# Kernel optimization log

Measured on AMD Instinct MI355X. Metric: run time of the kernel, lower is better.

Reference implementation:

```python
import jax, jax.numpy as jnp
import numpy as np

T, B, NIN, NOUT, NLAYER = 512, 32, 512, 1024, 2


def setup_inputs() -> dict:
    key = jax.random.key(0)
    ks = jax.random.split(key, 7)
    s = 0.02
    return {
        "x": jax.random.normal(ks[0], (T, B, NIN), dtype=jnp.float32),
        "h0": jax.random.normal(ks[1], (NLAYER, B, NOUT), dtype=jnp.float32),
        "c0": jax.random.normal(ks[2], (NLAYER, B, NOUT), dtype=jnp.float32),
        "W0": jax.random.normal(ks[3], (4 * NOUT, NIN + NOUT), dtype=jnp.float32) * s,
        "b0": jax.random.normal(ks[4], (4 * NOUT,), dtype=jnp.float32) * s,
        "W1": jax.random.normal(ks[5], (4 * NOUT, NOUT + NOUT), dtype=jnp.float32) * s,
        "b1": jax.random.normal(ks[6], (4 * NOUT,), dtype=jnp.float32) * s,
    }


def _cell(xt, ht, ct, W, b):
    # xt: [B, nin_l], ht/ct: [B, nout]
    z = jnp.concatenate([xt, ht], axis=1) @ W.T + b  # [B, 4*nout]
    g1, g2, g3, o = jnp.split(z, 4, axis=1)
    g1 = jax.nn.sigmoid(g1)
    g2 = jax.nn.sigmoid(g2)
    g3 = jax.nn.sigmoid(g3)
    o = jnp.tanh(o)
    ct1 = ct * g1 + o * g2
    ht1 = jnp.tanh(ct1) * g3
    return ht1, ct1


def reference(x, h0, c0, W0, b0, W1, b1):
    Ws, bs = (W0, W1), (b0, b1)

    def step(carry, xt):
        hs, cs = carry  # tuples of [B, nout]
        new_hs, new_cs = [], []
        inp = xt
        for i in range(NLAYER):
            h1, c1 = _cell(inp, hs[i], cs[i], Ws[i], bs[i])
            new_hs.append(h1)
            new_cs.append(c1)
            inp = h1
        return (tuple(new_hs), tuple(new_cs)), inp

    init = (tuple(h0[i] for i in range(NLAYER)), tuple(c0[i] for i in range(NLAYER)))
    _, outputs = jax.lax.scan(step, init, x)  # [T, B, nout]
    # Faithful to source: returns the ORIGINAL (h0, c0), not the final state.
    return outputs, (h0, c0)
```

## Files before the change

kernel.cpp:

```cpp
#include <hip/hip_runtime.h>
#include <hip/hip_bf16.h>

#define TSTEPS 512
#define BATCH  32
#define NIN    512
#define NH     1024
#define BNH    (BATCH * NH)

typedef __attribute__((ext_vector_type(8))) short  short8v;
typedef __attribute__((ext_vector_type(4))) float  float4v;
typedef unsigned long long ull;

__device__ __forceinline__ unsigned short f2bf(float f) {
  return __builtin_bit_cast(unsigned short, __float2bfloat16(f));
}
__device__ __forceinline__ float4v mfma16(short8v a, short8v b, float4v c) {
  return __builtin_amdgcn_mfma_f32_16x16x32_bf16(a, b, c, 0, 0, 0);
}

__device__ __forceinline__ int swzh(int b, int k) {
  return (k >> 5) * 1024 + (b >> 4) * 512 + ((k >> 2) & 1) * 256 +
         (((b & 15) | (((k >> 3) & 3) << 4)) << 2) + (k & 3);
}
__device__ __forceinline__ int swzx(int b, int k) {
  return (k >> 5) * 1024 + (b >> 4) * 512 +
         (((b & 15) | (((k >> 3) & 3) << 4)) << 3) + (k & 7);
}

template<bool X16>
__device__ __forceinline__ void kpart8(const ushort* __restrict__ base, int kgb,
                                       int lane, const short8v (&wreg)[8][2],
                                       float4v (&acc)[2][2]) {
  if constexpr (X16) {
    short8v f[2][8];
#pragma unroll
    for (int mt = 0; mt < 2; ++mt)
#pragma unroll
      for (int q = 0; q < 8; ++q)
        f[mt][q] = *(const short8v*)(base + (size_t)(kgb + q) * 1024 + mt * 512 + lane * 8);
#pragma unroll
    for (int q = 0; q < 8; ++q)
#pragma unroll
      for (int mt = 0; mt < 2; ++mt) {
        acc[mt][0] = mfma16(f[mt][q], wreg[q][0], acc[mt][0]);
        acc[mt][1] = mfma16(f[mt][q], wreg[q][1], acc[mt][1]);
      }
  } else {
    ull lo[2][8], hi[2][8];
#pragma unroll
    for (int mt = 0; mt < 2; ++mt)
#pragma unroll
      for (int q = 0; q < 8; ++q) {
        const ull* p = (const ull*)(base + (size_t)(kgb + q) * 1024 + mt * 512 + lane * 4);
        lo[mt][q] = __hip_atomic_load(p,      __ATOMIC_RELAXED, __HIP_MEMORY_SCOPE_SYSTEM);
        hi[mt][q] = __hip_atomic_load(p + 64, __ATOMIC_RELAXED, __HIP_MEMORY_SCOPE_SYSTEM);
      }
#pragma unroll
    for (int q = 0; q < 8; ++q)
#pragma unroll
      for (int mt = 0; mt < 2; ++mt) {
        union { ull u[2]; short8v v; } cv;
        cv.u[0] = lo[mt][q]; cv.u[1] = hi[mt][q];
        acc[mt][0] = mfma16(cv.v, wreg[q][0], acc[mt][0]);
        acc[mt][1] = mfma16(cv.v, wreg[q][1], acc[mt][1]);
      }
  }
}

__device__ __forceinline__ void wave_poll(const int* __restrict__ flags,
                                          int base, int cnt, int need, int lane) {
  if (need <= 0) return;
  const int* f = flags + (size_t)(base + (lane & (cnt - 1))) * 4;
  while (!__all(__hip_atomic_load(f, __ATOMIC_RELAXED, __HIP_MEMORY_SCOPE_SYSTEM) >= need)) {}
  asm volatile("" ::: "memory");
}

__global__ __launch_bounds__(512, 2)
void lstm_rs(const float* __restrict__ c0_in,
             const float* __restrict__ W0, const float* __restrict__ b0_,
             const float* __restrict__ W1, const float* __restrict__ b1_,
             const ushort* __restrict__ xbf,
             ushort* __restrict__ ring0,
             ushort* __restrict__ ring1,
             int* __restrict__ flags,
             float* __restrict__ out) {
  __shared__ float zl[8][32][33];

  const int wg    = blockIdx.x;
  const int tid   = threadIdx.x;
  const int res   = wg & 7;
  const int layer = res >> 2;
  const int rank  = (wg >> 3) * 4 + (res & 3);
  const int j0    = rank * 8;
  const int K     = layer ? (2 * NH) : (NIN + NH);
  const float* W    = layer ? W1 : W0;
  const float* bias = layer ? b1_ : b0_;

  const int wv = tid >> 6, lane = tid & 63;
  const bool kactive = layer ? true : (wv < 6);

  short8v wreg[8][2];
  if (kactive) {
    const int wkbase = wv * 256;
#pragma unroll
    for (int q = 0; q < 8; ++q)
#pragma unroll
      for (int nt = 0; nt < 2; ++nt) {
        int n  = nt * 16 + (lane & 15);
        int gr = (n >> 3) * NH + j0 + (n & 7);
        int k  = wkbase + q * 32 + (lane >> 4) * 8;
        const float* p = W + (size_t)gr * K + k;
        float4 f0 = *(const float4*)p;
        float4 f1 = *(const float4*)(p + 4);
        short8v r;
        r[0] = (short)f2bf(f0.x); r[1] = (short)f2bf(f0.y);
        r[2] = (short)f2bf(f0.z); r[3] = (short)f2bf(f0.w);
        r[4] = (short)f2bf(f1.x); r[5] = (short)f2bf(f1.y);
        r[6] = (short)f2bf(f1.z); r[7] = (short)f2bf(f1.w);
        wreg[q][nt] = r;
      }
  } else {
#pragma unroll
    for (int q = 0; q < 8; ++q) { wreg[q][0] = short8v{}; wreg[q][1] = short8v{}; }
  }

  for (int i = lane; i < 32 * 33; i += 64) (&zl[wv][0][0])[i] = 0.f;

  const int bb = tid >> 3, jj = tid & 7;
  float c = 0.f, bg0 = 0.f, bg1 = 0.f, bg2 = 0.f, bg3 = 0.f;
  if (tid < 256) {
    bg0 = bias[0 * NH + j0 + jj];
    bg1 = bias[1 * NH + j0 + jj];
    bg2 = bias[2 * NH + j0 + jj];
    bg3 = bias[3 * NH + j0 + jj];
    c   = c0_in[layer * BNH + bb * NH + j0 + jj];
  }

  __syncthreads();

  for (int it = 0; it < TSTEPS; ++it) {
    float4v acc[2][2] = {{{0,0,0,0},{0,0,0,0}},{{0,0,0,0},{0,0,0,0}}};

    if (layer == 0) {
      if (wv < 2) {
        kpart8<true>(xbf + (size_t)it * 16384, 8 * wv, lane, wreg, acc);
      } else if (wv < 6) {
        wave_poll(flags, 32 * (wv - 2), 32, it, lane);
        kpart8<false>(ring0 + (size_t)(it & 7) * BNH, 8 * (wv - 2), lane, wreg, acc);
      } else {
        wave_poll(flags, 128 + 64 * (wv - 6), 64, it - 6, lane);
      }
    } else {
      if (wv < 4) {
        wave_poll(flags, 32 * wv, 32, it + 1, lane);
        kpart8<false>(ring0 + (size_t)((it + 1) & 7) * BNH, 8 * wv, lane, wreg, acc);
      } else {
        wave_poll(flags, 128 + 32 * (wv - 4), 32, it, lane);
        kpart8<false>(ring1 + (size_t)((it + 1) & 1) * BNH, 8 * (wv - 4), lane, wreg, acc);
      }
    }

    if (kactive) {
#pragma unroll
      for (int mt = 0; mt < 2; ++mt)
#pragma unroll
        for (int nt = 0; nt < 2; ++nt)
#pragma unroll
          for (int r = 0; r < 4; ++r)
            zl[wv][mt * 16 + (lane >> 4) * 4 + r][nt * 16 + (lane & 15)] = acc[mt][nt][r];
    }
    __syncthreads();

    if (tid < 256) {
      float zg[4];
#pragma unroll
      for (int g = 0; g < 4; ++g) {
        float s = 0.f;
#pragma unroll
        for (int w = 0; w < 8; ++w) s += zl[w][bb][g * 8 + jj];
        zg[g] = s;
      }
      float g1 = 1.f / (1.f + __expf(-(zg[0] + bg0)));
      float g2 = 1.f / (1.f + __expf(-(zg[1] + bg1)));
      float g3 = 1.f / (1.f + __expf(-(zg[2] + bg2)));
      float o  = tanhf(zg[3] + bg3);
      c = c * g1 + o * g2;
      float h = tanhf(c) * g3;
      unsigned short hb = f2bf(h);
      int so = swzh(bb, j0 + jj);
      if (layer == 0) {
        __hip_atomic_store(&ring0[(size_t)((it + 1) & 7) * BNH + so], hb,
                           __ATOMIC_RELAXED, __HIP_MEMORY_SCOPE_SYSTEM);
      } else {
        __hip_atomic_store(&ring1[(size_t)(it & 1) * BNH + so], hb,
                           __ATOMIC_RELAXED, __HIP_MEMORY_SCOPE_SYSTEM);
        out[(size_t)it * BNH + bb * NH + j0 + jj] = h;
      }
    }
    asm volatile("s_waitcnt vmcnt(0)" ::: "memory");
    __syncthreads();
    if (tid == 0) {
      __hip_atomic_store(&flags[(size_t)(layer * 128 + rank) * 4], it + 1,
                         __ATOMIC_RELAXED, __HIP_MEMORY_SCOPE_SYSTEM);
    }
  }
}

__global__ void prep(const float* __restrict__ x,
                     const float* __restrict__ h0_in, const float* __restrict__ c0_in,
                     ushort* __restrict__ xbf, ushort* __restrict__ ring0,
                     ushort* __restrict__ ring1, int* __restrict__ flags,
                     float* __restrict__ out) {
  int i = blockIdx.x * blockDim.x + threadIdx.x;
  {
    int t = i >> 14, rem = i & 16383;
    int b = rem >> 9, k = rem & 511;
    xbf[(size_t)t * 16384 + swzx(b, k)] = f2bf(x[i]);
  }
  if (i < BNH) {
    int b = i >> 10, j = i & 1023;
    int so = swzh(b, j);
    __hip_atomic_store(&ring0[so], f2bf(h0_in[i]),
                       __ATOMIC_RELAXED, __HIP_MEMORY_SCOPE_SYSTEM);
    __hip_atomic_store(&ring1[BNH + so], f2bf(h0_in[BNH + i]),
                       __ATOMIC_RELAXED, __HIP_MEMORY_SCOPE_SYSTEM);
  }
  if (i < 1024) {
    __hip_atomic_store(&flags[i], 0, __ATOMIC_RELAXED, __HIP_MEMORY_SCOPE_SYSTEM);
  }
  if (i < 2 * BNH) {
    const size_t TB = (size_t)TSTEPS * BNH;
    out[TB + i]           = h0_in[i];
    out[TB + 2 * BNH + i] = c0_in[i];
  }
}

extern "C" void kernel_launch(void* const* d_in, const int* in_sizes, int n_in,
                              void* d_out, int out_size, void* d_ws, size_t ws_size,
                              hipStream_t stream) {
  const float* x  = (const float*)d_in[0];
  const float* h0 = (const float*)d_in[1];
  const float* c0 = (const float*)d_in[2];
  const float* W0 = (const float*)d_in[3];
  const float* b0 = (const float*)d_in[4];
  const float* W1 = (const float*)d_in[5];
  const float* b1 = (const float*)d_in[6];
  float* out = (float*)d_out;

  ushort* xbf   = (ushort*)d_ws;
  ushort* ring0 = (ushort*)((char*)d_ws + 16777216);
  ushort* ring1 = (ushort*)((char*)d_ws + 17301504);
  int*    flags = (int*)((char*)d_ws + 17432576);

  prep<<<dim3(32768), dim3(256), 0, stream>>>(x, h0, c0, xbf, ring0, ring1, flags, out);

  void* args[] = {(void*)&c0, (void*)&W0, (void*)&b0, (void*)&W1, (void*)&b1,
                  (void*)&xbf, (void*)&ring0, (void*)&ring1, (void*)&flags, (void*)&out};
  (void)hipLaunchCooperativeKernel((const void*)lstm_rs, dim3(256), dim3(512),
                                   args, 0, stream);
}
```

Before: 2.778 ms.

## Replace ring buffers with full-history buffer and block-level flag polling

Layer 0 hidden states now go into a full per-timestep bf16 buffer instead of an 8-slot ring, and layer 1 reads its own previous output straight from the fp32 output tensor, converting on the fly. The x-to-bf16 prep pass is dropped; x is read as fp32 and converted inside the recurrent kernel. Per-wave polling with atomic loads is replaced by one wave polling all 128 flags with s_sleep, followed by a block barrier, and flags are spaced 64 bytes apart to cut contention. The change removes the big prep kernel and the ring-slot throttle between layers, at the cost of extra fp32 loads and conversions on the critical path and a barrier per step.

```diff
diff --git a/kernel.cpp b/kernel.cpp
--- a/kernel.cpp
+++ b/kernel.cpp
@@ -9,7 +9,6 @@
 
 typedef __attribute__((ext_vector_type(8))) short  short8v;
 typedef __attribute__((ext_vector_type(4))) float  float4v;
-typedef unsigned long long ull;
 
 __device__ __forceinline__ unsigned short f2bf(float f) {
   return __builtin_bit_cast(unsigned short, __float2bfloat16(f));
@@ -18,73 +17,83 @@
   return __builtin_amdgcn_mfma_f32_16x16x32_bf16(a, b, c, 0, 0, 0);
 }
 
-__device__ __forceinline__ int swzh(int b, int k) {
-  return (k >> 5) * 1024 + (b >> 4) * 512 + ((k >> 2) & 1) * 256 +
-         (((b & 15) | (((k >> 3) & 3) << 4)) << 2) + (k & 3);
-}
 __device__ __forceinline__ int swzx(int b, int k) {
   return (k >> 5) * 1024 + (b >> 4) * 512 +
          (((b & 15) | (((k >> 3) & 3) << 4)) << 3) + (k & 7);
 }
 
-template<bool X16>
-__device__ __forceinline__ void kpart8(const ushort* __restrict__ base, int kgb,
+__device__ __forceinline__ short8v cvt8(float4 f0, float4 f1) {
+  short8v r;
+  r[0] = (short)f2bf(f0.x); r[1] = (short)f2bf(f0.y);
+  r[2] = (short)f2bf(f0.z); r[3] = (short)f2bf(f0.w);
+  r[4] = (short)f2bf(f1.x); r[5] = (short)f2bf(f1.y);
+  r[6] = (short)f2bf(f1.z); r[7] = (short)f2bf(f1.w);
+  return r;
+}
+
+__device__ __forceinline__ void kpartB(const ushort* __restrict__ base, int kgb,
                                        int lane, const short8v (&wreg)[8][2],
                                        float4v (&acc)[2][2]) {
-  if constexpr (X16) {
-    short8v f[2][8];
-#pragma unroll
-    for (int mt = 0; mt < 2; ++mt)
-#pragma unroll
-      for (int q = 0; q < 8; ++q)
-        f[mt][q] = *(const short8v*)(base + (size_t)(kgb + q) * 1024 + mt * 512 + lane * 8);
+  short8v f[2][8];
+#pragma unroll
+  for (int mt = 0; mt < 2; ++mt)
 #pragma unroll
     for (int q = 0; q < 8; ++q)
-#pragma unroll
-      for (int mt = 0; mt < 2; ++mt) {
-        acc[mt][0] = mfma16(f[mt][q], wreg[q][0], acc[mt][0]);
-        acc[mt][1] = mfma16(f[mt][q], wreg[q][1], acc[mt][1]);
-      }
-  } else {
-    ull lo[2][8], hi[2][8];
-#pragma unroll
-    for (int mt = 0; mt < 2; ++mt)
-#pragma unroll
-      for (int q = 0; q < 8; ++q) {
-        const ull* p = (const ull*)(base + (size_t)(kgb + q) * 1024 + mt * 512 + lane * 4);
-        lo[mt][q] = __hip_atomic_load(p,      __ATOMIC_RELAXED, __HIP_MEMORY_SCOPE_SYSTEM);
-        hi[mt][q] = __hip_atomic_load(p + 64, __ATOMIC_RELAXED, __HIP_MEMORY_SCOPE_SYSTEM);
-      }
-#pragma unroll
-    for (int q = 0; q < 8; ++q)
-#pragma unroll
-      for (int mt = 0; mt < 2; ++mt) {
-        union { ull u[2]; short8v v; } cv;
-        cv.u[0] = lo[mt][q]; cv.u[1] = hi[mt][q];
-        acc[mt][0] = mfma16(cv.v, wreg[q][0], acc[mt][0]);
-        acc[mt][1] = mfma16(cv.v, wreg[q][1], acc[mt][1]);
-      }
-  }
-}
-
-__device__ __forceinline__ void wave_poll(const int* __restrict__ flags,
-                                          int base, int cnt, int need, int lane) {
+      f[mt][q] = *(const short8v*)(base + (size_t)(kgb + q) * 1024 + mt * 512 + lane * 8);
+#pragma unroll
+  for (int q = 0; q < 8; ++q)
+#pragma unroll
+    for (int mt = 0; mt < 2; ++mt) {
+      acc[mt][0] = mfma16(f[mt][q], wreg[q][0], acc[mt][0]);
+      acc[mt][1] = mfma16(f[mt][q], wreg[q][1], acc[mt][1]);
+    }
+}
+
+template<int RS>
+__device__ __forceinline__ void kpartF(const float* __restrict__ base, int kgb,
+                                       int lane, const short8v (&wreg)[8][2],
+                                       float4v (&acc)[2][2]) {
+  const int r0 = lane & 15, koff = (lane >> 4) * 8;
+  short8v f[2][8];
+#pragma unroll
+  for (int mt = 0; mt < 2; ++mt)
+#pragma unroll
+    for (int q = 0; q < 8; ++q) {
+      const float* p = base + (size_t)(mt * 16 + r0) * RS + (kgb + q) * 32 + koff;
+      f[mt][q] = cvt8(*(const float4*)p, *(const float4*)(p + 4));
+    }
+#pragma unroll
+  for (int q = 0; q < 8; ++q)
+#pragma unroll
+    for (int mt = 0; mt < 2; ++mt) {
+      acc[mt][0] = mfma16(f[mt][q], wreg[q][0], acc[mt][0]);
+      acc[mt][1] = mfma16(f[mt][q], wreg[q][1], acc[mt][1]);
+    }
+}
+
+__device__ __forceinline__ void poll128(const int* __restrict__ flags, int base,
+                                        int need, int lane) {
   if (need <= 0) return;
-  const int* f = flags + (size_t)(base + (lane & (cnt - 1))) * 4;
-  while (!__all(__hip_atomic_load(f, __ATOMIC_RELAXED, __HIP_MEMORY_SCOPE_SYSTEM) >= need)) {}
-  asm volatile("" ::: "memory");
+  const int* fa = flags + (size_t)(base + lane) * 16;
+  const int* fb = flags + (size_t)(base + 64 + lane) * 16;
+  for (;;) {
+    int a = __hip_atomic_load(fa, __ATOMIC_RELAXED, __HIP_MEMORY_SCOPE_SYSTEM);
+    int b = __hip_atomic_load(fb, __ATOMIC_RELAXED, __HIP_MEMORY_SCOPE_SYSTEM);
+    if (__all((a >= need) && (b >= need))) break;
+    __builtin_amdgcn_s_sleep(1);
+  }
 }
 
 __global__ __launch_bounds__(512, 2)
-void lstm_rs(const float* __restrict__ c0_in,
+void lstm_ch(const float* __restrict__ x,
+             const float* __restrict__ h0_in,
+             const float* __restrict__ c0_in,
              const float* __restrict__ W0, const float* __restrict__ b0_,
              const float* __restrict__ W1, const float* __restrict__ b1_,
-             const ushort* __restrict__ xbf,
              ushort* __restrict__ ring0,
-             ushort* __restrict__ ring1,
              int* __restrict__ flags,
              float* __restrict__ out) {
-  __shared__ float zl[8][32][33];
+  __shared__ float zl[8][32][36];
 
   const int wg    = blockIdx.x;
   const int tid   = threadIdx.x;
@@ -110,21 +119,14 @@
         int gr = (n >> 3) * NH + j0 + (n & 7);
         int k  = wkbase + q * 32 + (lane >> 4) * 8;
         const float* p = W + (size_t)gr * K + k;
-        float4 f0 = *(const float4*)p;
-        float4 f1 = *(const float4*)(p + 4);
-        short8v r;
-        r[0] = (short)f2bf(f0.x); r[1] = (short)f2bf(f0.y);
-        r[2] = (short)f2bf(f0.z); r[3] = (short)f2bf(f0.w);
-        r[4] = (short)f2bf(f1.x); r[5] = (short)f2bf(f1.y);
-        r[6] = (short)f2bf(f1.z); r[7] = (short)f2bf(f1.w);
-        wreg[q][nt] = r;
+        wreg[q][nt] = cvt8(*(const float4*)p, *(const float4*)(p + 4));
       }
   } else {
 #pragma unroll
     for (int q = 0; q < 8; ++q) { wreg[q][0] = short8v{}; wreg[q][1] = short8v{}; }
   }
 
-  for (int i = lane; i < 32 * 33; i += 64) (&zl[wv][0][0])[i] = 0.f;
+  for (int i = lane; i < 32 * 36; i += 64) (&zl[wv][0][0])[i] = 0.f;
 
   const int bb = tid >> 3, jj = tid & 7;
   float c = 0.f, bg0 = 0.f, bg1 = 0.f, bg2 = 0.f, bg3 = 0.f;
@@ -139,24 +141,28 @@
   __syncthreads();
 
   for (int it = 0; it < TSTEPS; ++it) {
+    if (layer == 0) {
+      if (wv == 2) poll128(flags, 0, it, lane);
+    } else {
+      if (wv == 0) poll128(flags, 0, it + 1, lane);
+      if (wv == 4) poll128(flags, 128, it, lane);
+    }
+    __syncthreads();
+    asm volatile("" ::: "memory");
+
     float4v acc[2][2] = {{{0,0,0,0},{0,0,0,0}},{{0,0,0,0},{0,0,0,0}}};
-
     if (layer == 0) {
       if (wv < 2) {
-        kpart8<true>(xbf + (size_t)it * 16384, 8 * wv, lane, wreg, acc);
+        kpartF<NIN>(x + (size_t)it * BATCH * NIN, 8 * wv, lane, wreg, acc);
       } else if (wv < 6) {
-        wave_poll(flags, 32 * (wv - 2), 32, it, lane);
-        kpart8<false>(ring0 + (size_t)(it & 7) * BNH, 8 * (wv - 2), lane, wreg, acc);
-      } else {
-        wave_poll(flags, 128 + 64 * (wv - 6), 64, it - 6, lane);
+        kpartB(ring0 + (size_t)it * BNH, 8 * (wv - 2), lane, wreg, acc);
       }
     } else {
       if (wv < 4) {
-        wave_poll(flags, 32 * wv, 32, it + 1, lane);
-        kpart8<false>(ring0 + (size_t)((it + 1) & 7) * BNH, 8 * wv, lane, wreg, acc);
+        kpartB(ring0 + (size_t)(it + 1) * BNH, 8 * wv, lane, wreg, acc);
       } else {
-        wave_poll(flags, 128 + 32 * (wv - 4), 32, it, lane);
-        kpart8<false>(ring1 + (size_t)((it + 1) & 1) * BNH, 8 * (wv - 4), lane, wreg, acc);
+        const float* h1b = it ? (out + (size_t)(it - 1) * BNH) : (h0_in + BNH);
+        kpartF<NH>(h1b, 8 * (wv - 4), lane, wreg, acc);
       }
     }
 
@@ -186,53 +192,38 @@
       float o  = tanhf(zg[3] + bg3);
       c = c * g1 + o * g2;
       float h = tanhf(c) * g3;
-      unsigned short hb = f2bf(h);
-      int so = swzh(bb, j0 + jj);
       if (layer == 0) {
-        __hip_atomic_store(&ring0[(size_t)((it + 1) & 7) * BNH + so], hb,
+        __hip_atomic_store(&ring0[(size_t)(it + 1) * BNH + swzx(bb, j0 + jj)],
+                           f2bf(h), __ATOMIC_RELAXED, __HIP_MEMORY_SCOPE_SYSTEM);
+      } else {
+        __hip_atomic_store(&out[(size_t)it * BNH + bb * NH + j0 + jj], h,
                            __ATOMIC_RELAXED, __HIP_MEMORY_SCOPE_SYSTEM);
-      } else {
-        __hip_atomic_store(&ring1[(size_t)(it & 1) * BNH + so], hb,
-                           __ATOMIC_RELAXED, __HIP_MEMORY_SCOPE_SYSTEM);
-        out[(size_t)it * BNH + bb * NH + j0 + jj] = h;
       }
     }
     asm volatile("s_waitcnt vmcnt(0)" ::: "memory");
     __syncthreads();
     if (tid == 0) {
-      __hip_atomic_store(&flags[(size_t)(layer * 128 + rank) * 4], it + 1,
+      __hip_atomic_store(&flags[(size_t)(layer * 128 + rank) * 16], it + 1,
                          __ATOMIC_RELAXED, __HIP_MEMORY_SCOPE_SYSTEM);
     }
   }
 }
 
-__global__ void prep(const float* __restrict__ x,
-                     const float* __restrict__ h0_in, const float* __restrict__ c0_in,
-                     ushort* __restrict__ xbf, ushort* __restrict__ ring0,
-                     ushort* __restrict__ ring1, int* __restrict__ flags,
+__global__ void prep(const float* __restrict__ h0_in, const float* __restrict__ c0_in,
+                     ushort* __restrict__ ring0, int* __restrict__ flags,
                      float* __restrict__ out) {
   int i = blockIdx.x * blockDim.x + threadIdx.x;
-  {
-    int t = i >> 14, rem = i & 16383;
-    int b = rem >> 9, k = rem & 511;
-    xbf[(size_t)t * 16384 + swzx(b, k)] = f2bf(x[i]);
-  }
   if (i < BNH) {
     int b = i >> 10, j = i & 1023;
-    int so = swzh(b, j);
-    __hip_atomic_store(&ring0[so], f2bf(h0_in[i]),
+    __hip_atomic_store(&ring0[swzx(b, j)], f2bf(h0_in[i]),
                        __ATOMIC_RELAXED, __HIP_MEMORY_SCOPE_SYSTEM);
-    __hip_atomic_store(&ring1[BNH + so], f2bf(h0_in[BNH + i]),
-                       __ATOMIC_RELAXED, __HIP_MEMORY_SCOPE_SYSTEM);
-  }
-  if (i < 1024) {
+  }
+  if (i < 256 * 16) {
     __hip_atomic_store(&flags[i], 0, __ATOMIC_RELAXED, __HIP_MEMORY_SCOPE_SYSTEM);
   }
-  if (i < 2 * BNH) {
-    const size_t TB = (size_t)TSTEPS * BNH;
-    out[TB + i]           = h0_in[i];
-    out[TB + 2 * BNH + i] = c0_in[i];
-  }
+  const size_t TB = (size_t)TSTEPS * BNH;
+  out[TB + i]           = h0_in[i];
+  out[TB + 2 * BNH + i] = c0_in[i];
 }
 
 extern "C" void kernel_launch(void* const* d_in, const int* in_sizes, int n_in,
@@ -247,15 +238,13 @@
   const float* b1 = (const float*)d_in[6];
   float* out = (float*)d_out;
 
-  ushort* xbf   = (ushort*)d_ws;
-  ushort* ring0 = (ushort*)((char*)d_ws + 16777216);
-  ushort* ring1 = (ushort*)((char*)d_ws + 17301504);
-  int*    flags = (int*)((char*)d_ws + 17432576);
-
-  prep<<<dim3(32768), dim3(256), 0, stream>>>(x, h0, c0, xbf, ring0, ring1, flags, out);
-
-  void* args[] = {(void*)&c0, (void*)&W0, (void*)&b0, (void*)&W1, (void*)&b1,
-                  (void*)&xbf, (void*)&ring0, (void*)&ring1, (void*)&flags, (void*)&out};
-  (void)hipLaunchCooperativeKernel((const void*)lstm_rs, dim3(256), dim3(512),
+  ushort* ring0 = (ushort*)d_ws;
+  int*    flags = (int*)((char*)d_ws + (size_t)(TSTEPS + 1) * BNH * 2);
+
+  prep<<<dim3(256), dim3(256), 0, stream>>>(h0, c0, ring0, flags, out);
+
+  void* args[] = {(void*)&x, (void*)&h0, (void*)&c0, (void*)&W0, (void*)&b0,
+                  (void*)&W1, (void*)&b1, (void*)&ring0, (void*)&flags, (void*)&out};
+  (void)hipLaunchCooperativeKernel((const void*)lstm_ch, dim3(256), dim3(512),
                                    args, 0, stream);
 }
```

After: 4.236 ms. 52.5% more time.

## Software-pipeline LSTM step with triple-buffered gate LDS and per-wave flags

Applied to the files above, without the earlier changes.

Restructures the persistent LSTM loop so the gate nonlinearity for step it-1 runs in the same iteration as the GEMM loads for step it, using a triple-buffered LDS accumulator and a single barrier per iteration. Per-wave flags, each padded to its own cache line, replace the single per-block flag published after a second barrier. Polling now checks two flags per lane with s_sleep backoff, and the hidden-state ring uses the x swizzle so reads become contiguous 16-byte chunks. The goal is to cut barrier and flag latency on the serial recurrence critical path, at the cost of more LDS and more flag traffic.

```diff
diff --git a/kernel.cpp b/kernel.cpp
--- a/kernel.cpp
+++ b/kernel.cpp
@@ -18,73 +18,84 @@
   return __builtin_amdgcn_mfma_f32_16x16x32_bf16(a, b, c, 0, 0, 0);
 }
 
-__device__ __forceinline__ int swzh(int b, int k) {
-  return (k >> 5) * 1024 + (b >> 4) * 512 + ((k >> 2) & 1) * 256 +
-         (((b & 15) | (((k >> 3) & 3) << 4)) << 2) + (k & 3);
-}
 __device__ __forceinline__ int swzx(int b, int k) {
   return (k >> 5) * 1024 + (b >> 4) * 512 +
          (((b & 15) | (((k >> 3) & 3) << 4)) << 3) + (k & 7);
 }
 
-template<bool X16>
-__device__ __forceinline__ void kpart8(const ushort* __restrict__ base, int kgb,
-                                       int lane, const short8v (&wreg)[8][2],
-                                       float4v (&acc)[2][2]) {
-  if constexpr (X16) {
-    short8v f[2][8];
-#pragma unroll
-    for (int mt = 0; mt < 2; ++mt)
-#pragma unroll
-      for (int q = 0; q < 8; ++q)
-        f[mt][q] = *(const short8v*)(base + (size_t)(kgb + q) * 1024 + mt * 512 + lane * 8);
+__device__ __forceinline__ short8v cvt8(float4 f0, float4 f1) {
+  short8v r;
+  r[0] = (short)f2bf(f0.x); r[1] = (short)f2bf(f0.y);
+  r[2] = (short)f2bf(f0.z); r[3] = (short)f2bf(f0.w);
+  r[4] = (short)f2bf(f1.x); r[5] = (short)f2bf(f1.y);
+  r[6] = (short)f2bf(f1.z); r[7] = (short)f2bf(f1.w);
+  return r;
+}
+
+__device__ __forceinline__ void kload_b(const ushort* __restrict__ base, int lane,
+                                        short8v (&f)[2][8]) {
+#pragma unroll
+  for (int mt = 0; mt < 2; ++mt)
+#pragma unroll
+    for (int q = 0; q < 8; ++q) {
+      const ull* p = (const ull*)(base + q * 1024 + mt * 512 + lane * 8);
+      ull lo = __hip_atomic_load(p,     __ATOMIC_RELAXED, __HIP_MEMORY_SCOPE_SYSTEM);
+      ull hi = __hip_atomic_load(p + 1, __ATOMIC_RELAXED, __HIP_MEMORY_SCOPE_SYSTEM);
+      union { ull u[2]; short8v v; } cv;
+      cv.u[0] = lo; cv.u[1] = hi;
+      f[mt][q] = cv.v;
+    }
+}
+
+__device__ __forceinline__ void kloadp(const ushort* __restrict__ base, int lane,
+                                       short8v (&f)[2][8]) {
+#pragma unroll
+  for (int mt = 0; mt < 2; ++mt)
 #pragma unroll
     for (int q = 0; q < 8; ++q)
-#pragma unroll
-      for (int mt = 0; mt < 2; ++mt) {
-        acc[mt][0] = mfma16(f[mt][q], wreg[q][0], acc[mt][0]);
-        acc[mt][1] = mfma16(f[mt][q], wreg[q][1], acc[mt][1]);
-      }
-  } else {
-    ull lo[2][8], hi[2][8];
-#pragma unroll
-    for (int mt = 0; mt < 2; ++mt)
-#pragma unroll
-      for (int q = 0; q < 8; ++q) {
-        const ull* p = (const ull*)(base + (size_t)(kgb + q) * 1024 + mt * 512 + lane * 4);
-        lo[mt][q] = __hip_atomic_load(p,      __ATOMIC_RELAXED, __HIP_MEMORY_SCOPE_SYSTEM);
-        hi[mt][q] = __hip_atomic_load(p + 64, __ATOMIC_RELAXED, __HIP_MEMORY_SCOPE_SYSTEM);
-      }
-#pragma unroll
-    for (int q = 0; q < 8; ++q)
-#pragma unroll
-      for (int mt = 0; mt < 2; ++mt) {
-        union { ull u[2]; short8v v; } cv;
-        cv.u[0] = lo[mt][q]; cv.u[1] = hi[mt][q];
-        acc[mt][0] = mfma16(cv.v, wreg[q][0], acc[mt][0]);
-        acc[mt][1] = mfma16(cv.v, wreg[q][1], acc[mt][1]);
-      }
-  }
-}
-
-__device__ __forceinline__ void wave_poll(const int* __restrict__ flags,
-                                          int base, int cnt, int need, int lane) {
+      f[mt][q] = *(const short8v*)(base + q * 1024 + mt * 512 + lane * 8);
+}
+
+__device__ __forceinline__ void kmfma(const short8v (&f)[2][8],
+                                      const short8v (&w)[8][2],
+                                      float4v (&acc)[2][2]) {
+#pragma unroll
+  for (int q = 0; q < 8; ++q)
+#pragma unroll
+    for (int mt = 0; mt < 2; ++mt) {
+      acc[mt][0] = mfma16(f[mt][q], w[q][0], acc[mt][0]);
+      acc[mt][1] = mfma16(f[mt][q], w[q][1], acc[mt][1]);
+    }
+}
+
+template<int PL>
+__device__ __forceinline__ void wpoll(const int* __restrict__ flags, int base,
+                                      int need, int lane) {
   if (need <= 0) return;
-  const int* f = flags + (size_t)(base + (lane & (cnt - 1))) * 4;
-  while (!__all(__hip_atomic_load(f, __ATOMIC_RELAXED, __HIP_MEMORY_SCOPE_SYSTEM) >= need)) {}
+  const int* p0 = &flags[(size_t)(base + lane * PL) * 16];
+  for (;;) {
+    int mn = 0x7fffffff;
+#pragma unroll
+    for (int j = 0; j < PL; ++j) {
+      int v = __hip_atomic_load(p0 + j * 16, __ATOMIC_RELAXED, __HIP_MEMORY_SCOPE_SYSTEM);
+      mn = v < mn ? v : mn;
+    }
+    if (__all(mn >= need)) break;
+    __builtin_amdgcn_s_sleep(1);
+  }
   asm volatile("" ::: "memory");
 }
 
 __global__ __launch_bounds__(512, 2)
-void lstm_rs(const float* __restrict__ c0_in,
-             const float* __restrict__ W0, const float* __restrict__ b0_,
-             const float* __restrict__ W1, const float* __restrict__ b1_,
-             const ushort* __restrict__ xbf,
-             ushort* __restrict__ ring0,
-             ushort* __restrict__ ring1,
-             int* __restrict__ flags,
-             float* __restrict__ out) {
-  __shared__ float zl[8][32][33];
+void lstm_v10(const ushort* __restrict__ xbf,
+              const float* __restrict__ c0_in,
+              const float* __restrict__ W0, const float* __restrict__ b0_,
+              const float* __restrict__ W1, const float* __restrict__ b1_,
+              ushort* __restrict__ ring0,
+              ushort* __restrict__ ring1,
+              int* __restrict__ flags,
+              float* __restrict__ out) {
+  __shared__ float zl[3][8][32][36];
 
   const int wg    = blockIdx.x;
   const int tid   = threadIdx.x;
@@ -97,11 +108,12 @@
   const float* bias = layer ? b1_ : b0_;
 
   const int wv = tid >> 6, lane = tid & 63;
-  const bool kactive = layer ? true : (wv < 6);
+  const int kslot = layer ? wv : (wv < 2 ? wv : wv - 2);
+  const bool kact = layer || wv < 2 || wv >= 4;
 
   short8v wreg[8][2];
-  if (kactive) {
-    const int wkbase = wv * 256;
+  if (kact) {
+    const int wkbase = kslot * 256;
 #pragma unroll
     for (int q = 0; q < 8; ++q)
 #pragma unroll
@@ -110,21 +122,15 @@
         int gr = (n >> 3) * NH + j0 + (n & 7);
         int k  = wkbase + q * 32 + (lane >> 4) * 8;
         const float* p = W + (size_t)gr * K + k;
-        float4 f0 = *(const float4*)p;
-        float4 f1 = *(const float4*)(p + 4);
-        short8v r;
-        r[0] = (short)f2bf(f0.x); r[1] = (short)f2bf(f0.y);
-        r[2] = (short)f2bf(f0.z); r[3] = (short)f2bf(f0.w);
-        r[4] = (short)f2bf(f1.x); r[5] = (short)f2bf(f1.y);
-        r[6] = (short)f2bf(f1.z); r[7] = (short)f2bf(f1.w);
-        wreg[q][nt] = r;
+        wreg[q][nt] = cvt8(*(const float4*)p, *(const float4*)(p + 4));
       }
   } else {
 #pragma unroll
     for (int q = 0; q < 8; ++q) { wreg[q][0] = short8v{}; wreg[q][1] = short8v{}; }
   }
 
-  for (int i = lane; i < 32 * 33; i += 64) (&zl[wv][0][0])[i] = 0.f;
+  for (int b3 = 0; b3 < 3; ++b3)
+    for (int i = lane; i < 32 * 36; i += 64) (&zl[b3][wv][0][0])[i] = 0.f;
 
   const int bb = tid >> 3, jj = tid & 7;
   float c = 0.f, bg0 = 0.f, bg1 = 0.f, bg2 = 0.f, bg3 = 0.f;
@@ -138,46 +144,31 @@
 
   __syncthreads();
 
-  for (int it = 0; it < TSTEPS; ++it) {
-    float4v acc[2][2] = {{{0,0,0,0},{0,0,0,0}},{{0,0,0,0},{0,0,0,0}}};
-
-    if (layer == 0) {
-      if (wv < 2) {
-        kpart8<true>(xbf + (size_t)it * 16384, 8 * wv, lane, wreg, acc);
-      } else if (wv < 6) {
-        wave_poll(flags, 32 * (wv - 2), 32, it, lane);
-        kpart8<false>(ring0 + (size_t)(it & 7) * BNH, 8 * (wv - 2), lane, wreg, acc);
+  for (int it = 0; it <= TSTEPS; ++it) {
+    const bool gemm = (it < TSTEPS);
+    short8v f[2][8];
+
+    if (gemm && wv >= 4) {
+      const int i = wv - 4;
+      if (layer == 0) {
+        wpoll<2>(flags, 128 * i, it, lane);
+        kload_b(ring0 + (size_t)(it & 7) * BNH + 8 * i * 1024, lane, f);
       } else {
-        wave_poll(flags, 128 + 64 * (wv - 6), 64, it - 6, lane);
-      }
-    } else {
-      if (wv < 4) {
-        wave_poll(flags, 32 * wv, 32, it + 1, lane);
-        kpart8<false>(ring0 + (size_t)((it + 1) & 7) * BNH, 8 * wv, lane, wreg, acc);
-      } else {
-        wave_poll(flags, 128 + 32 * (wv - 4), 32, it, lane);
-        kpart8<false>(ring1 + (size_t)((it + 1) & 1) * BNH, 8 * (wv - 4), lane, wreg, acc);
-      }
-    }
-
-    if (kactive) {
-#pragma unroll
-      for (int mt = 0; mt < 2; ++mt)
-#pragma unroll
-        for (int nt = 0; nt < 2; ++nt)
-#pragma unroll
-          for (int r = 0; r < 4; ++r)
-            zl[wv][mt * 16 + (lane >> 4) * 4 + r][nt * 16 + (lane & 15)] = acc[mt][nt][r];
-    }
-    __syncthreads();
-
-    if (tid < 256) {
+        wpoll<2>(flags, 512 + 128 * i, it, lane);
+        kload_b(ring1 + (size_t)((it + 1) & 1) * BNH + 8 * i * 1024, lane, f);
+      }
+    }
+    if (layer == 0 && wv < 4) {
+      wpoll<2>(flags, 512 + 128 * wv, it - 6, lane);
+    }
+    if (it >= 1 && tid < 256) {
+      const int zb = (it + 2) % 3;
       float zg[4];
 #pragma unroll
       for (int g = 0; g < 4; ++g) {
         float s = 0.f;
 #pragma unroll
-        for (int w = 0; w < 8; ++w) s += zl[w][bb][g * 8 + jj];
+        for (int w = 0; w < 8; ++w) s += zl[zb][w][bb][g * 8 + jj];
         zg[g] = s;
       }
       float g1 = 1.f / (1.f + __expf(-(zg[0] + bg0)));
@@ -187,22 +178,45 @@
       c = c * g1 + o * g2;
       float h = tanhf(c) * g3;
       unsigned short hb = f2bf(h);
-      int so = swzh(bb, j0 + jj);
+      int so = swzx(bb, j0 + jj);
       if (layer == 0) {
-        __hip_atomic_store(&ring0[(size_t)((it + 1) & 7) * BNH + so], hb,
+        __hip_atomic_store(&ring0[(size_t)(it & 7) * BNH + so], hb,
                            __ATOMIC_RELAXED, __HIP_MEMORY_SCOPE_SYSTEM);
       } else {
-        __hip_atomic_store(&ring1[(size_t)(it & 1) * BNH + so], hb,
+        __hip_atomic_store(&ring1[(size_t)((it + 1) & 1) * BNH + so], hb,
                            __ATOMIC_RELAXED, __HIP_MEMORY_SCOPE_SYSTEM);
-        out[(size_t)it * BNH + bb * NH + j0 + jj] = h;
-      }
-    }
-    asm volatile("s_waitcnt vmcnt(0)" ::: "memory");
-    __syncthreads();
-    if (tid == 0) {
-      __hip_atomic_store(&flags[(size_t)(layer * 128 + rank) * 4], it + 1,
-                         __ATOMIC_RELAXED, __HIP_MEMORY_SCOPE_SYSTEM);
-    }
+      }
+      asm volatile("s_waitcnt vmcnt(0)" ::: "memory");
+      if (lane == 0) {
+        __hip_atomic_store(&flags[(size_t)((layer * 128 + rank) * 4 + wv) * 16], it,
+                           __ATOMIC_RELAXED, __HIP_MEMORY_SCOPE_SYSTEM);
+      }
+      if (layer == 1)
+        out[(size_t)(it - 1) * BNH + bb * NH + j0 + jj] = h;
+    }
+    if (gemm && wv < 4) {
+      if (layer == 0) {
+        if (wv < 2) kloadp(xbf + (size_t)it * 16384 + 8 * wv * 1024, lane, f);
+      } else {
+        wpoll<2>(flags, 128 * wv, it + 1, lane);
+        kload_b(ring0 + (size_t)((it + 1) & 7) * BNH + 8 * wv * 1024, lane, f);
+      }
+    }
+    if (gemm && kact) {
+      float4v acc[2][2] = {{{0,0,0,0},{0,0,0,0}},{{0,0,0,0},{0,0,0,0}}};
+      kmfma(f, wreg, acc);
+      const int zc = it % 3;
+#pragma unroll
+      for (int mt = 0; mt < 2; ++mt)
+#pragma unroll
+        for (int nt = 0; nt < 2; ++nt)
+#pragma unroll
+          for (int r = 0; r < 4; ++r)
+            zl[zc][wv][mt * 16 + (lane >> 4) * 4 + r][nt * 16 + (lane & 15)] = acc[mt][nt][r];
+    }
+    asm volatile("s_waitcnt lgkmcnt(0)" ::: "memory");
+    __builtin_amdgcn_s_barrier();
+    asm volatile("" ::: "memory");
   }
 }
 
@@ -219,13 +233,13 @@
   }
   if (i < BNH) {
     int b = i >> 10, j = i & 1023;
-    int so = swzh(b, j);
+    int so = swzx(b, j);
     __hip_atomic_store(&ring0[so], f2bf(h0_in[i]),
                        __ATOMIC_RELAXED, __HIP_MEMORY_SCOPE_SYSTEM);
     __hip_atomic_store(&ring1[BNH + so], f2bf(h0_in[BNH + i]),
                        __ATOMIC_RELAXED, __HIP_MEMORY_SCOPE_SYSTEM);
   }
-  if (i < 1024) {
+  if (i < 1024 * 16) {
     __hip_atomic_store(&flags[i], 0, __ATOMIC_RELAXED, __HIP_MEMORY_SCOPE_SYSTEM);
   }
   if (i < 2 * BNH) {
@@ -254,8 +268,8 @@
 
   prep<<<dim3(32768), dim3(256), 0, stream>>>(x, h0, c0, xbf, ring0, ring1, flags, out);
 
-  void* args[] = {(void*)&c0, (void*)&W0, (void*)&b0, (void*)&W1, (void*)&b1,
-                  (void*)&xbf, (void*)&ring0, (void*)&ring1, (void*)&flags, (void*)&out};
-  (void)hipLaunchCooperativeKernel((const void*)lstm_rs, dim3(256), dim3(512),
+  void* args[] = {(void*)&xbf, (void*)&c0, (void*)&W0, (void*)&b0, (void*)&W1,
+                  (void*)&b1, (void*)&ring0, (void*)&ring1, (void*)&flags, (void*)&out};
+  (void)hipLaunchCooperativeKernel((const void*)lstm_v10, dim3(256), dim3(512),
                                    args, 0, stream);
 }
```

Result: slower. 8.686 ms (+212.7%).
